# Kernel tuning notes

Measured on AMD Instinct MI355X. Metric: run time of the kernel, lower is better.

Reference implementation:

```python
import jax, jax.numpy as jnp
import numpy as np

N_NODES = 50000
N_EDGES = 800000
N_GRAPHS = 1024
NODE_IN = 128
HID = 300
DEPTH = 5
READOUT = 1024


def setup_inputs() -> dict:
    key = jax.random.key(0)
    ks = jax.random.split(key, 12)
    x = jax.random.normal(ks[0], (N_NODES, NODE_IN), dtype=jnp.float32)
    edge_index = jax.random.randint(ks[1], (2, N_EDGES), 0, N_NODES, dtype=jnp.int32)
    batch = jnp.sort(jax.random.randint(ks[2], (N_NODES,), 0, N_GRAPHS, dtype=jnp.int32))
    s_in = 1.0 / np.sqrt(NODE_IN)
    s_h = 1.0 / np.sqrt(HID)
    W_proj = jax.random.normal(ks[3], (NODE_IN, HID), dtype=jnp.float32) * s_in
    b_proj = jnp.zeros((HID,), dtype=jnp.float32)
    W1 = jax.random.normal(ks[4], (DEPTH, HID, HID), dtype=jnp.float32) * s_h
    b1 = jnp.zeros((DEPTH, HID), dtype=jnp.float32)
    W2 = jax.random.normal(ks[5], (DEPTH, HID, HID), dtype=jnp.float32) * s_h
    b2 = jnp.zeros((DEPTH, HID), dtype=jnp.float32)
    W_sp = jax.random.normal(ks[6], (HID, READOUT), dtype=jnp.float32) * s_h
    b_sp = jnp.zeros((READOUT,), dtype=jnp.float32)
    prelu_a = jnp.full((1,), 0.25, dtype=jnp.float32)  # nn.PReLU default
    return {"x": x, "edge_index": edge_index, "batch": batch,
            "W_proj": W_proj, "b_proj": b_proj, "W1": W1, "b1": b1,
            "W2": W2, "b2": b2, "W_sp": W_sp, "b_sp": b_sp, "prelu_a": prelu_a}


def reference(x, edge_index, batch, W_proj, b_proj, W1, b1, W2, b2, W_sp, b_sp, prelu_a):
    # project_node_feats: Linear + ReLU
    h = jax.nn.relu(x @ W_proj + b_proj)  # [N, HID]
    src = edge_index[0]
    dst = edge_index[1]
    for i in range(DEPTH):
        # GINConv (eps=0): out = nn(x + sum_{j in N(i)} x_j)
        agg = h + jax.ops.segment_sum(h[src], dst, num_segments=N_NODES)
        h = jax.nn.relu(agg @ W1[i] + b1[i]) @ W2[i] + b2[i]
        if i < DEPTH - 1:
            h = jax.nn.relu(h)
        # dropout is identity in eval mode
    # global_add_pool over graph ids
    pooled = jax.ops.segment_sum(h, batch, num_segments=N_GRAPHS)  # [G, HID]
    z = pooled @ W_sp + b_sp  # [G, READOUT]
    # PReLU with single shared parameter
    readout = jnp.where(z >= 0, z, prelu_a[0] * z)
    return readout
```

## Files before the change

### kernel.cpp

```cpp
#include <hip/hip_runtime.h>
#include <cstdint>

#define N_NODES 50000
#define N_EDGES 800000
#define N_GRAPHS 1024
#define NODE_IN 128
#define HID 300
#define DEPTH 5
#define READOUT 1024
#define PSTR 320
#define XSTR 384

typedef float f32x4 __attribute__((ext_vector_type(4)));
typedef short bf16x8 __attribute__((ext_vector_type(8)));
typedef unsigned short us8 __attribute__((ext_vector_type(8)));

__device__ inline unsigned short f2bf(float v) {
    unsigned u = __float_as_uint(v);
    unsigned r = u + 0x7FFFu + ((u >> 16) & 1u);
    return (unsigned short)(r >> 16);
}
__device__ inline float bf2f(unsigned short h) {
    return __uint_as_float((unsigned)h << 16);
}
__device__ inline float bflo(unsigned u) { return __uint_as_float(u << 16); }
__device__ inline float bfhi(unsigned u) { return __uint_as_float(u & 0xFFFF0000u); }
__device__ inline unsigned packbf(float a, float b) {
    return (unsigned)f2bf(a) | ((unsigned)f2bf(b) << 16);
}

__global__ void hist2(const int* __restrict__ dst, int* __restrict__ cnt,
                      const int* __restrict__ batch, int* __restrict__ gcnt) {
    int i = blockIdx.x * blockDim.x + threadIdx.x;
    if (i < N_EDGES) atomicAdd(&cnt[dst[i]], 1);
    else if (i < N_EDGES + N_NODES) atomicAdd(&gcnt[batch[i - N_EDGES]], 1);
}

__global__ __launch_bounds__(256)
void scan_block2(const int* __restrict__ cnt, int* __restrict__ offs, int* __restrict__ bsum,
                 const int* __restrict__ gcnt, int* __restrict__ goffs, int* __restrict__ gsum,
                 int nbn) {
    __shared__ int buf[256];
    int b = blockIdx.x;
    const int* in; int* out; int* bs; int n; int bi;
    if (b < nbn) { in = cnt; out = offs; bs = bsum; n = N_NODES; bi = b; }
    else { in = gcnt; out = goffs; bs = gsum; n = N_GRAPHS; bi = b - nbn; }
    int i = bi * 256 + (int)threadIdx.x;
    int v = (i < n) ? in[i] : 0;
    buf[threadIdx.x] = v;
    __syncthreads();
    for (int off = 1; off < 256; off <<= 1) {
        int t = ((int)threadIdx.x >= off) ? buf[threadIdx.x - off] : 0;
        __syncthreads();
        buf[threadIdx.x] += t;
        __syncthreads();
    }
    if (i < n) out[i] = buf[threadIdx.x] - v;
    if (threadIdx.x == 255) bs[bi] = buf[255];
}

__global__ __launch_bounds__(256)
void scan_base2(const int* __restrict__ bsum, int* __restrict__ bbase, int nbn, int* __restrict__ tot_n,
                const int* __restrict__ gsum, int* __restrict__ gbase, int nbg, int* __restrict__ tot_g) {
    __shared__ int buf[256];
    const int* bs; int* bb; int nb; int* tot;
    if (blockIdx.x == 0) { bs = bsum; bb = bbase; nb = nbn; tot = tot_n; }
    else { bs = gsum; bb = gbase; nb = nbg; tot = tot_g; }
    int v = ((int)threadIdx.x < nb) ? bs[threadIdx.x] : 0;
    buf[threadIdx.x] = v;
    __syncthreads();
    for (int off = 1; off < 256; off <<= 1) {
        int t = ((int)threadIdx.x >= off) ? buf[threadIdx.x - off] : 0;
        __syncthreads();
        buf[threadIdx.x] += t;
        __syncthreads();
    }
    if ((int)threadIdx.x < nb) bb[threadIdx.x] = buf[threadIdx.x] - v;
    if (threadIdx.x == 255) *tot = buf[255];
}

__global__ void scan_add2(int* __restrict__ offs, const int* __restrict__ bbase,
                          int* __restrict__ cursor,
                          int* __restrict__ goffs, const int* __restrict__ gbase, int nbn) {
    int b = blockIdx.x;
    if (b < nbn) {
        int i = b * 256 + (int)threadIdx.x;
        if (i < N_NODES) {
            int o = offs[i] + bbase[b];
            offs[i] = o;
            cursor[i] = o;
        }
    } else {
        int bi = b - nbn;
        int i = bi * 256 + (int)threadIdx.x;
        if (i < N_GRAPHS) goffs[i] += gbase[bi];
    }
}

__global__ void scatter_kernel(const int* __restrict__ src, const int* __restrict__ dst,
                               int* __restrict__ cursor, int* __restrict__ csr, int n) {
    int i = blockIdx.x * blockDim.x + threadIdx.x;
    if (i < n) {
        int p = atomicAdd(&cursor[dst[i]], 1);
        csr[p] = src[i];
    }
}

__global__ __launch_bounds__(256)
void aggregate_bf16(const unsigned short* __restrict__ h, const int* __restrict__ offs,
                    const int* __restrict__ csr, unsigned short* __restrict__ out) {
    int wave = (int)((blockIdx.x * blockDim.x + threadIdx.x) >> 6);
    int lane = threadIdx.x & 63;
    if (wave >= N_NODES) return;
    float a0, a1, a2, a3, a4, a5;
    {
        const unsigned* r = (const unsigned*)(h + (size_t)wave * PSTR);
        uint2 u = *(const uint2*)&r[2 * lane];
        unsigned t = (lane < 32) ? r[128 + lane] : 0u;
        a0 = bflo(u.x); a1 = bfhi(u.x);
        a2 = bflo(u.y); a3 = bfhi(u.y);
        a4 = bflo(t);   a5 = bfhi(t);
    }
    int s = offs[wave], e = offs[wave + 1];
    int k = s;
    for (; k + 3 < e; k += 4) {
        const unsigned* r0 = (const unsigned*)(h + (size_t)csr[k] * PSTR);
        const unsigned* r1 = (const unsigned*)(h + (size_t)csr[k + 1] * PSTR);
        const unsigned* r2 = (const unsigned*)(h + (size_t)csr[k + 2] * PSTR);
        const unsigned* r3 = (const unsigned*)(h + (size_t)csr[k + 3] * PSTR);
        uint2 x0 = *(const uint2*)&r0[2 * lane];
        uint2 x1 = *(const uint2*)&r1[2 * lane];
        uint2 x2 = *(const uint2*)&r2[2 * lane];
        uint2 x3 = *(const uint2*)&r3[2 * lane];
        unsigned t0 = 0, t1 = 0, t2 = 0, t3 = 0;
        if (lane < 32) {
            t0 = r0[128 + lane]; t1 = r1[128 + lane];
            t2 = r2[128 + lane]; t3 = r3[128 + lane];
        }
        a0 += bflo(x0.x) + bflo(x1.x) + bflo(x2.x) + bflo(x3.x);
        a1 += bfhi(x0.x) + bfhi(x1.x) + bfhi(x2.x) + bfhi(x3.x);
        a2 += bflo(x0.y) + bflo(x1.y) + bflo(x2.y) + bflo(x3.y);
        a3 += bfhi(x0.y) + bfhi(x1.y) + bfhi(x2.y) + bfhi(x3.y);
        a4 += bflo(t0) + bflo(t1) + bflo(t2) + bflo(t3);
        a5 += bfhi(t0) + bfhi(t1) + bfhi(t2) + bfhi(t3);
    }
    for (; k < e; ++k) {
        const unsigned* r = (const unsigned*)(h + (size_t)csr[k] * PSTR);
        uint2 u = *(const uint2*)&r[2 * lane];
        unsigned t = (lane < 32) ? r[128 + lane] : 0u;
        a0 += bflo(u.x); a1 += bfhi(u.x);
        a2 += bflo(u.y); a3 += bfhi(u.y);
        a4 += bflo(t);   a5 += bfhi(t);
    }
    unsigned* o = (unsigned*)(out + (size_t)wave * PSTR);
    uint2 w; w.x = packbf(a0, a1); w.y = packbf(a2, a3);
    *(uint2*)&o[2 * lane] = w;
    if (lane < 32) o[128 + lane] = (lane < 22) ? packbf(a4, a5) : 0u;
}

__global__ __launch_bounds__(256)
void split_all(const float* __restrict__ W1, const float* __restrict__ W2,
               const float* __restrict__ Wsp, const float* __restrict__ Wproj,
               unsigned short* __restrict__ w1S, unsigned short* __restrict__ w2S,
               unsigned short* __restrict__ spH, unsigned short* __restrict__ spL,
               unsigned short* __restrict__ Bp) {
    __shared__ float tile[32][33];
    const int STK_SZ = 320 * 640;
    int z = blockIdx.z;
    const float* W;
    int K, N;
    if (z < 10) {
        if (blockIdx.x >= 10) return;
        int l = z % 5;
        W = (z < 5 ? W1 : W2) + (size_t)l * HID * HID;
        K = HID; N = HID;
    } else if (z == 10) {
        W = Wsp; K = HID; N = READOUT;
    } else {
        if (blockIdx.x >= 10 || blockIdx.y >= 4) return;
        W = Wproj; K = NODE_IN; N = HID;
    }
    int n0 = blockIdx.x * 32, k0 = blockIdx.y * 32;
    int tx = threadIdx.x & 31, ty = threadIdx.x >> 5;
#pragma unroll
    for (int r = 0; r < 4; ++r) {
        int k = k0 + ty + r * 8, n = n0 + tx;
        tile[ty + r * 8][tx] = (k < K && n < N) ? W[(size_t)k * N + n] : 0.f;
    }
    __syncthreads();
#pragma unroll
    for (int r = 0; r < 4; ++r) {
        int n = n0 + ty + r * 8, k = k0 + tx;
        float v = tile[tx][ty + r * 8];
        unsigned short hb = f2bf(v);
        unsigned short lb = f2bf(v - bf2f(hb));
        if (z < 10) {
            unsigned short* S = (z < 5 ? w1S : w2S) + (size_t)(z % 5) * STK_SZ;
            S[(size_t)n * 640 + k] = hb;
            S[(size_t)n * 640 + 320 + k] = lb;
        } else if (z == 10) {
            spH[(size_t)n * 320 + k] = hb;
            spL[(size_t)n * 320 + k] = lb;
        } else {
            Bp[(size_t)n * XSTR + k] = hb;
            Bp[(size_t)n * XSTR + 128 + k] = hb;
            Bp[(size_t)n * XSTR + 256 + k] = lb;
        }
    }
}

__global__ void split_x(const float* __restrict__ x, unsigned short* __restrict__ xs) {
    int i = blockIdx.x * blockDim.x + threadIdx.x;
    if (i >= N_NODES * 64) return;
    int row = i >> 6, c = i & 63;
    float2 v = *(const float2*)&x[(size_t)row * NODE_IN + 2 * c];
    unsigned short h0 = f2bf(v.x), h1 = f2bf(v.y);
    unsigned short l0 = f2bf(v.x - bf2f(h0)), l1 = f2bf(v.y - bf2f(h1));
    unsigned hp = (unsigned)h0 | ((unsigned)h1 << 16);
    unsigned lp = (unsigned)l0 | ((unsigned)l1 << 16);
    unsigned* o = (unsigned*)(xs + (size_t)row * XSTR);
    o[c] = hp;
    o[64 + c] = lp;
    o[128 + c] = hp;
}

#define BSWZ(r, c) ((c) ^ (((r) >> 1) & 3))

__global__ __launch_bounds__(256, 2)
void gin_mlp64(const unsigned short* __restrict__ Ap, int M,
               const unsigned short* __restrict__ B1, const float* __restrict__ b1,
               const unsigned short* __restrict__ B2, const float* __restrict__ b2,
               unsigned short* __restrict__ Op, int act2) {
    __shared__ __align__(16) unsigned short At[64 * 320];
    __shared__ __align__(16) unsigned short Bs[2 * 10240];

    const int tid = threadIdx.x;
    const int bm = blockIdx.x * 64;
    const int wn = tid >> 6, lane = tid & 63;
    const int lr = lane & 15, lk = lane >> 4;

    float b1v[5], b2v[5];
#pragma unroll
    for (int n = 0; n < 5; ++n) {
        int col = wn * 80 + n * 16 + lr;
        b1v[n] = (col < HID) ? b1[col] : 0.f;
        b2v[n] = (col < HID) ? b2[col] : 0.f;
    }

    size_t bofs[10]; int bldso[10];
#pragma unroll
    for (int i = 0; i < 10; ++i) {
        int q = i * 256 + tid;
        int half = q >= 1280;
        int q2 = q - half * 1280;
        int r = q2 >> 2, c = q2 & 3;
        bofs[i] = (size_t)r * 640 + half * 320 + c * 8;
        bldso[i] = half * 10240 + r * 32 + BSWZ(r, c) * 8;
    }

    us8 vB[10];
    auto LOADB = [&](const unsigned short* B, int t) {
        int k0 = t * 32;
#pragma unroll
        for (int i = 0; i < 10; ++i)
            vB[i] = *(const us8*)&B[bofs[i] + k0];
    };

    LOADB(B1, 0);

#pragma unroll
    for (int i = 0; i < 10; ++i) {
        int g = i * 256 + tid;
        int row = g / 40, c = g - row * 40;
        int grow = bm + row; if (grow >= M) grow = M - 1;
        us8 v = *(const us8*)&Ap[(size_t)grow * PSTR + c * 8];
        *(us8*)&At[row * 320 + (c ^ (row & 7)) * 8] = v;
    }

    f32x4 acc[4][5];

    auto RUN = [&](const unsigned short* B) {
        for (int t = 0; t < 10; ++t) {
            __syncthreads();
#pragma unroll
            for (int i = 0; i < 10; ++i) *(us8*)&Bs[bldso[i]] = vB[i];
            if (t < 9) LOADB(B, t + 1);
            __syncthreads();
            bf16x8 aS[4];
            int ac = t * 4 + lk;
#pragma unroll
            for (int m = 0; m < 4; ++m) {
                int row = m * 16 + lr;
                aS[m] = *(const bf16x8*)&At[row * 320 + (ac ^ (row & 7)) * 8];
            }
#pragma unroll
            for (int n = 0; n < 5; ++n) {
                int rb = wn * 80 + n * 16 + lr;
                int sc = rb * 32 + BSWZ(rb, lk) * 8;
                bf16x8 bh = *(const bf16x8*)&Bs[sc];
                bf16x8 bl = *(const bf16x8*)&Bs[10240 + sc];
#pragma unroll
                for (int m = 0; m < 4; ++m) {
                    acc[m][n] = __builtin_amdgcn_mfma_f32_16x16x32_bf16(aS[m], bh, acc[m][n], 0, 0, 0);
                    acc[m][n] = __builtin_amdgcn_mfma_f32_16x16x32_bf16(aS[m], bl, acc[m][n], 0, 0, 0);
                }
            }
        }
    };

#pragma unroll
    for (int m = 0; m < 4; ++m)
#pragma unroll
        for (int n = 0; n < 5; ++n) acc[m][n] = (f32x4)0.f;
    RUN(B1);

    LOADB(B2, 0);

    __syncthreads();
#pragma unroll
    for (int n = 0; n < 5; ++n) {
        int col = wn * 80 + n * 16 + lr;
        int cc = col >> 3, cp = col & 7;
        float bv = b1v[n];
        bool vc = col < HID;
#pragma unroll
        for (int m = 0; m < 4; ++m) {
#pragma unroll
            for (int p = 0; p < 4; ++p) {
                int row = m * 16 + lk * 4 + p;
                float v = vc ? fmaxf(acc[m][n][p] + bv, 0.f) : 0.f;
                At[row * 320 + ((cc ^ (row & 7)) * 8) + cp] = f2bf(v);
            }
        }
    }

#pragma unroll
    for (int m = 0; m < 4; ++m)
#pragma unroll
        for (int n = 0; n < 5; ++n) acc[m][n] = (f32x4)0.f;
    RUN(B2);

    __syncthreads();
#pragma unroll
    for (int n = 0; n < 5; ++n) {
        int col = wn * 80 + n * 16 + lr;
        int cc = col >> 3, cp = col & 7;
        float bv = b2v[n];
        bool vc = col < HID;
#pragma unroll
        for (int m = 0; m < 4; ++m) {
#pragma unroll
            for (int p = 0; p < 4; ++p) {
                int row = m * 16 + lk * 4 + p;
                float v = vc ? (acc[m][n][p] + bv) : 0.f;
                if (act2) v = fmaxf(v, 0.f);
                At[row * 320 + ((cc ^ (row & 7)) * 8) + cp] = f2bf(v);
            }
        }
    }
    __syncthreads();
#pragma unroll
    for (int i = 0; i < 10; ++i) {
        int g = i * 256 + tid;
        int row = g / 40, c = g - row * 40;
        int grow = bm + row;
        if (grow < M)
            *(us8*)&Op[(size_t)grow * PSTR + c * 8] =
                *(const us8*)&At[row * 320 + (c ^ (row & 7)) * 8];
    }
}

template<int NPL>
__global__ __launch_bounds__(512)
void gemm_plane4(const unsigned short* __restrict__ Ap, int astr, int M, int KP,
                 const unsigned short* __restrict__ BH, const unsigned short* __restrict__ BL,
                 const float* __restrict__ bias, unsigned short* __restrict__ Op, int act) {
    constexpr int BITER = (NPL * 1280 + 511) / 512;
    __shared__ __align__(16) unsigned short As[2][256 * 40];
    __shared__ __align__(16) unsigned short Bs[2][NPL * 10240];

    const int tid = threadIdx.x;
    const int bm = blockIdx.x * 256;
    const int wid = tid >> 6, lane = tid & 63;
    const int wm = wid >> 2, wn = wid & 3;
    const int lr = lane & 15, lk = lane >> 4;
    const int arow = tid >> 1, ach = (tid & 1) * 2;
    int agr = bm + arow; if (agr >= M) agr = M - 1;
    const unsigned short* aSrc = Ap + (size_t)agr * astr + ach * 8;

    const unsigned short* bsrc[BITER];
    int bldso[BITER];
    bool bval[BITER];
#pragma unroll
    for (int i = 0; i < BITER; ++i) {
        int qq = i * 512 + tid;
        bval[i] = qq < NPL * 1280;
        int p = (NPL == 2 && qq >= 1280) ? 1 : 0;
        int q2 = qq - p * 1280;
        int r = q2 >> 2, c = q2 & 3;
        const unsigned short* base = p ? BL : BH;
        bsrc[i] = base + (size_t)r * KP + c * 8;
        bldso[i] = p * 10240 + r * 32 + BSWZ(r, c) * 8;
    }

    f32x4 acc[8][5];
#pragma unroll
    for (int m = 0; m < 8; ++m)
#pragma unroll
        for (int n = 0; n < 5; ++n) acc[m][n] = (f32x4)0.f;

    us8 vA0, vA1, vB[BITER];
    auto LOADS = [&](int t) {
        int k0 = t * 32;
        vA0 = *(const us8*)&aSrc[k0];
        vA1 = *(const us8*)&aSrc[k0 + 8];
#pragma unroll
        for (int i = 0; i < BITER; ++i)
            if (bval[i]) vB[i] = *(const us8*)&bsrc[i][k0];
    };
    auto WRITE = [&](int b) {
        *(us8*)&As[b][arow * 40 + ach * 8] = vA0;
        *(us8*)&As[b][arow * 40 + ach * 8 + 8] = vA1;
#pragma unroll
        for (int i = 0; i < BITER; ++i)
            if (bval[i]) *(us8*)&Bs[b][bldso[i]] = vB[i];
    };

    const int nt = KP / 32;
    LOADS(0);
    WRITE(0);
    int buf = 0;
    for (int t = 0; t < nt; ++t) {
        bool more = (t + 1 < nt);
        if (more) LOADS(t + 1);
        __syncthreads();
        bf16x8 aS[8];
#pragma unroll
        for (int m = 0; m < 8; ++m)
            aS[m] = *(const bf16x8*)&As[buf][(wm * 128 + m * 16 + lr) * 40 + lk * 8];
#pragma unroll
        for (int n = 0; n < 5; ++n) {
            int rb = wn * 80 + n * 16 + lr;
            int sc = rb * 32 + BSWZ(rb, lk) * 8;
            bf16x8 bh = *(const bf16x8*)&Bs[buf][sc];
#pragma unroll
            for (int m = 0; m < 8; ++m)
                acc[m][n] = __builtin_amdgcn_mfma_f32_16x16x32_bf16(aS[m], bh, acc[m][n], 0, 0, 0);
            if (NPL == 2) {
                bf16x8 bl = *(const bf16x8*)&Bs[buf][10240 + sc];
#pragma unroll
                for (int m = 0; m < 8; ++m)
                    acc[m][n] = __builtin_amdgcn_mfma_f32_16x16x32_bf16(aS[m], bl, acc[m][n], 0, 0, 0);
            }
        }
        if (more) WRITE(buf ^ 1);
        buf ^= 1;
    }
#pragma unroll
    for (int n = 0; n < 5; ++n) {
        int col = wn * 80 + n * 16 + lr;
        bool vc = col < HID;
        float bv = vc ? bias[col] : 0.f;
#pragma unroll
        for (int m = 0; m < 8; ++m) {
            int rbase = bm + wm * 128 + m * 16 + lk * 4;
#pragma unroll
            for (int p = 0; p < 4; ++p) {
                int row = rbase + p;
                if (row >= M) continue;
                float v = vc ? (acc[m][n][p] + bv) : 0.f;
                if (act == 1) v = fmaxf(v, 0.f);
                Op[(size_t)row * PSTR + col] = f2bf(v);
            }
        }
    }
}

__global__ __launch_bounds__(256)
void gemm_f32A(const float* __restrict__ A, int lda, int M, int K, int KP,
               const unsigned short* __restrict__ BH, const unsigned short* __restrict__ BL, int KPB,
               const float* __restrict__ bias, int N,
               float* __restrict__ C, int ldc, int act, const float* __restrict__ prelu) {
    __shared__ __align__(16) unsigned short AsH[64 * 40];
    __shared__ __align__(16) unsigned short AsL[64 * 40];
    __shared__ __align__(16) unsigned short BsH[320 * 40];
    __shared__ __align__(16) unsigned short BsL[320 * 40];

    const int tid = threadIdx.x;
    const int bm = blockIdx.y * 64;
    const int bn = blockIdx.x * 320;
    const int wid = tid >> 6, lane = tid & 63;
    const int lr = lane & 15, lk = lane >> 4;
    const int ar = tid >> 2, ac = tid & 3;

    f32x4 acc[4][5];
#pragma unroll
    for (int m = 0; m < 4; ++m)
#pragma unroll
        for (int n = 0; n < 5; ++n) acc[m][n] = (f32x4)0.f;

    for (int k0 = 0; k0 < KP; k0 += 32) {
        {
            int gm = bm + ar;
            int k = k0 + ac * 8;
            float v[8];
#pragma unroll
            for (int j = 0; j < 8; ++j) v[j] = 0.f;
            if (gm < M) {
                if (k + 7 < K) {
                    float4 p0 = *(const float4*)&A[(size_t)gm * lda + k];
                    float4 p1 = *(const float4*)&A[(size_t)gm * lda + k + 4];
                    v[0] = p0.x; v[1] = p0.y; v[2] = p0.z; v[3] = p0.w;
                    v[4] = p1.x; v[5] = p1.y; v[6] = p1.z; v[7] = p1.w;
                } else {
#pragma unroll
                    for (int j = 0; j < 8; ++j)
                        if (k + j < K) v[j] = A[(size_t)gm * lda + k + j];
                }
            }
            us8 h, l;
#pragma unroll
            for (int j = 0; j < 8; ++j) {
                unsigned short hb = f2bf(v[j]);
                h[j] = hb;
                l[j] = f2bf(v[j] - bf2f(hb));
            }
            *(us8*)&AsH[ar * 40 + ac * 8] = h;
            *(us8*)&AsL[ar * 40 + ac * 8] = l;
        }
#pragma unroll
        for (int p = 0; p < 5; ++p) {
            int r = ar + p * 64;
            size_t gb = (size_t)(bn + r) * KPB + k0 + ac * 8;
            *(us8*)&BsH[r * 40 + ac * 8] = *(const us8*)&BH[gb];
            *(us8*)&BsL[r * 40 + ac * 8] = *(const us8*)&BL[gb];
        }
        __syncthreads();
        bf16x8 aH[4], aL[4];
#pragma unroll
        for (int m = 0; m < 4; ++m) {
            aH[m] = *(const bf16x8*)&AsH[(m * 16 + lr) * 40 + lk * 8];
            aL[m] = *(const bf16x8*)&AsL[(m * 16 + lr) * 40 + lk * 8];
        }
#pragma unroll
        for (int n = 0; n < 5; ++n) {
            int r = wid * 80 + n * 16 + lr;
            bf16x8 bh = *(const bf16x8*)&BsH[r * 40 + lk * 8];
            bf16x8 bl = *(const bf16x8*)&BsL[r * 40 + lk * 8];
#pragma unroll
            for (int m = 0; m < 4; ++m) {
                acc[m][n] = __builtin_amdgcn_mfma_f32_16x16x32_bf16(aH[m], bh, acc[m][n], 0, 0, 0);
                acc[m][n] = __builtin_amdgcn_mfma_f32_16x16x32_bf16(aH[m], bl, acc[m][n], 0, 0, 0);
                acc[m][n] = __builtin_amdgcn_mfma_f32_16x16x32_bf16(aL[m], bh, acc[m][n], 0, 0, 0);
            }
        }
        __syncthreads();
    }
    float slope = (act == 2) ? prelu[0] : 0.f;
#pragma unroll
    for (int n = 0; n < 5; ++n) {
        int col = bn + wid * 80 + n * 16 + lr;
        bool vc = col < N;
        float bv = vc ? bias[col] : 0.f;
#pragma unroll
        for (int m = 0; m < 4; ++m) {
            int rbase = bm + m * 16 + lk * 4;
#pragma unroll
            for (int p = 0; p < 4; ++p) {
                int row = rbase + p;
                if (row >= M) continue;
                float v = vc ? (acc[m][n][p] + bv) : 0.f;
                if (act == 1) v = fmaxf(v, 0.f);
                else if (act == 2) v = (v >= 0.f) ? v : slope * v;
                if (vc) C[(size_t)row * ldc + col] = v;
            }
        }
    }
}

__global__ __launch_bounds__(128)
void pool_seg(const unsigned short* __restrict__ h, const int* __restrict__ goffs,
              float* __restrict__ pooled) {
    __shared__ float red[6 * 64];
    int g = blockIdx.x;
    int w = threadIdx.x >> 6, lane = threadIdx.x & 63;
    int s = goffs[g], e = goffs[g + 1];
    float a0 = 0.f, a1 = 0.f, a2 = 0.f, a3 = 0.f, a4 = 0.f, a5 = 0.f;
    for (int node = s + w; node < e; node += 2) {
        const unsigned* r = (const unsigned*)(h + (size_t)node * PSTR);
        uint2 u = *(const uint2*)&r[2 * lane];
        unsigned t = (lane < 32) ? r[128 + lane] : 0u;
        a0 += bflo(u.x); a1 += bfhi(u.x);
        a2 += bflo(u.y); a3 += bfhi(u.y);
        a4 += bflo(t);   a5 += bfhi(t);
    }
    if (w == 1) {
        red[lane] = a0;        red[64 + lane] = a1;
        red[128 + lane] = a2;  red[192 + lane] = a3;
        red[256 + lane] = a4;  red[320 + lane] = a5;
    }
    __syncthreads();
    if (w == 0) {
        a0 += red[lane];        a1 += red[64 + lane];
        a2 += red[128 + lane];  a3 += red[192 + lane];
        a4 += red[256 + lane];  a5 += red[320 + lane];
        float* pr = pooled + (size_t)g * PSTR;
        *(float4*)&pr[4 * lane] = make_float4(a0, a1, a2, a3);
        if (lane < 32) *(float2*)&pr[256 + 2 * lane] = make_float2(a4, a5);
    }
}

extern "C" void kernel_launch(void* const* d_in, const int* in_sizes, int n_in,
                              void* d_out, int out_size, void* d_ws, size_t ws_size,
                              hipStream_t stream) {
    const float* x      = (const float*)d_in[0];
    const int*   eidx   = (const int*)d_in[1];
    const int*   batch  = (const int*)d_in[2];
    const float* W_proj = (const float*)d_in[3];
    const float* b_proj = (const float*)d_in[4];
    const float* W1     = (const float*)d_in[5];
    const float* b1     = (const float*)d_in[6];
    const float* W2     = (const float*)d_in[7];
    const float* b2     = (const float*)d_in[8];
    const float* W_sp   = (const float*)d_in[9];
    const float* b_sp   = (const float*)d_in[10];
    const float* prelu  = (const float*)d_in[11];

    const int* src = eidx;
    const int* dst = eidx + N_EDGES;

    const size_t PLANE  = (size_t)N_NODES * PSTR + 64;
    const size_t XPLANE = (size_t)N_NODES * XSTR + 64;
    const int STK_SZ = 320 * 640;
    const int SP_SZ  = 1280 * 320;
    const int BP_SZ  = 320 * XSTR;
    const int NB  = (N_NODES + 255) / 256;
    const int NBG = (N_GRAPHS + 255) / 256;

    unsigned short* hA  = (unsigned short*)d_ws;
    unsigned short* hBx = hA + PLANE;
    unsigned short* xs  = hBx;
    float* pooled = (float*)(hBx + XPLANE);
    unsigned short* w1S = (unsigned short*)(pooled + (size_t)N_GRAPHS * PSTR + 16);
    unsigned short* w2S = w1S + 5 * (size_t)STK_SZ;
    unsigned short* spH = w2S + 5 * (size_t)STK_SZ;
    unsigned short* spL = spH + SP_SZ;
    unsigned short* Bp  = spL + SP_SZ;
    int* cnt    = (int*)(((uintptr_t)(Bp + BP_SZ) + 15) & ~(uintptr_t)15);
    int* gcnt   = cnt + N_NODES;
    int* bsum   = gcnt + N_GRAPHS;
    int* bbase  = bsum + 256;
    int* gsum   = bbase + 256;
    int* gbase  = gsum + 256;
    int* offs   = gbase + 256;
    int* goffs  = offs + N_NODES + 1;
    int* cursor = goffs + N_GRAPHS + 1;
    int* csr    = cursor + N_NODES;
    size_t needed = (size_t)((uintptr_t)(csr + N_EDGES) - (uintptr_t)d_ws);
    if (ws_size < needed) return;

    split_all<<<dim3(40, 10, 12), 256, 0, stream>>>(W1, W2, W_sp, W_proj,
                                                    w1S, w2S, spH, spL, Bp);
    split_x<<<(N_NODES * 64 + 255) / 256, 256, 0, stream>>>(x, xs);

    hipMemsetAsync(cnt, 0, (N_NODES + N_GRAPHS) * sizeof(int), stream);
    hist2<<<(N_EDGES + N_NODES + 255) / 256, 256, 0, stream>>>(dst, cnt, batch, gcnt);
    scan_block2<<<NB + NBG, 256, 0, stream>>>(cnt, offs, bsum, gcnt, goffs, gsum, NB);
    scan_base2<<<2, 256, 0, stream>>>(bsum, bbase, NB, offs + N_NODES,
                                      gsum, gbase, NBG, goffs + N_GRAPHS);
    scan_add2<<<NB + NBG, 256, 0, stream>>>(offs, bbase, cursor, goffs, gbase, NB);
    scatter_kernel<<<(N_EDGES + 255) / 256, 256, 0, stream>>>(src, dst, cursor, csr, N_EDGES);

    gemm_plane4<1><<<(N_NODES + 255) / 256, 512, 0, stream>>>(
        xs, XSTR, N_NODES, XSTR, Bp, nullptr, b_proj, hA, 1);

    const int GBM = (N_NODES + 63) / 64;
    unsigned short* cur = hA;
    unsigned short* agp = hBx;
    for (int i = 0; i < DEPTH; ++i) {
        aggregate_bf16<<<(N_NODES * 64 + 255) / 256, 256, 0, stream>>>(cur, offs, csr, agp);
        gin_mlp64<<<GBM, 256, 0, stream>>>(
            agp, N_NODES,
            w1S + (size_t)i * STK_SZ, b1 + (size_t)i * HID,
            w2S + (size_t)i * STK_SZ, b2 + (size_t)i * HID,
            cur, (i < DEPTH - 1) ? 1 : 0);
    }

    pool_seg<<<N_GRAPHS, 128, 0, stream>>>(cur, goffs, pooled);

    gemm_f32A<<<dim3(4, (N_GRAPHS + 63) / 64), 256, 0, stream>>>(
        pooled, PSTR, N_GRAPHS, HID, 320, spH, spL, 320,
        b_sp, READOUT, (float*)d_out, READOUT, 2, prelu);
}
```

Baseline: 1.031 ms.

## Enlarge GIN MLP tile to 128 rows and fuse fp32 projection GEMM

The fused GIN MLP kernel now handles 128 rows per block with 512 threads (8 waves in a 2x4 layout) and uses a K-step of 64 with a new XOR swizzle. Each weight tile loaded into LDS is therefore reused across twice as many rows, and the kernel needs fewer barriers. Separately, the input projection now reuses the fp32-A split GEMM directly on x, which removes the split_x preprocessing kernel and the padded x plane, and the GEMM gains a bf16 plane output mode. The larger LDS footprint (about 160KB) allows only one block per CU, which may hurt latency hiding, and the projection GEMM now uses a 64-row tile.

```diff
diff --git a/kernel.cpp b/kernel.cpp
--- a/kernel.cpp
+++ b/kernel.cpp
@@ -9,7 +9,6 @@
 #define DEPTH 5
 #define READOUT 1024
 #define PSTR 320
-#define XSTR 384
 
 typedef float f32x4 __attribute__((ext_vector_type(4)));
 typedef short bf16x8 __attribute__((ext_vector_type(8)));
@@ -163,7 +162,7 @@
                const float* __restrict__ Wsp, const float* __restrict__ Wproj,
                unsigned short* __restrict__ w1S, unsigned short* __restrict__ w2S,
                unsigned short* __restrict__ spH, unsigned short* __restrict__ spL,
-               unsigned short* __restrict__ Bp) {
+               unsigned short* __restrict__ pjH, unsigned short* __restrict__ pjL) {
     __shared__ float tile[32][33];
     const int STK_SZ = 320 * 640;
     int z = blockIdx.z;
@@ -202,41 +201,26 @@
             spH[(size_t)n * 320 + k] = hb;
             spL[(size_t)n * 320 + k] = lb;
         } else {
-            Bp[(size_t)n * XSTR + k] = hb;
-            Bp[(size_t)n * XSTR + 128 + k] = hb;
-            Bp[(size_t)n * XSTR + 256 + k] = lb;
-        }
-    }
-}
-
-__global__ void split_x(const float* __restrict__ x, unsigned short* __restrict__ xs) {
-    int i = blockIdx.x * blockDim.x + threadIdx.x;
-    if (i >= N_NODES * 64) return;
-    int row = i >> 6, c = i & 63;
-    float2 v = *(const float2*)&x[(size_t)row * NODE_IN + 2 * c];
-    unsigned short h0 = f2bf(v.x), h1 = f2bf(v.y);
-    unsigned short l0 = f2bf(v.x - bf2f(h0)), l1 = f2bf(v.y - bf2f(h1));
-    unsigned hp = (unsigned)h0 | ((unsigned)h1 << 16);
-    unsigned lp = (unsigned)l0 | ((unsigned)l1 << 16);
-    unsigned* o = (unsigned*)(xs + (size_t)row * XSTR);
-    o[c] = hp;
-    o[64 + c] = lp;
-    o[128 + c] = hp;
+            pjH[(size_t)n * 128 + k] = hb;
+            pjL[(size_t)n * 128 + k] = lb;
+        }
+    }
 }
 
 #define BSWZ(r, c) ((c) ^ (((r) >> 1) & 3))
 
-__global__ __launch_bounds__(256, 2)
-void gin_mlp64(const unsigned short* __restrict__ Ap, int M,
-               const unsigned short* __restrict__ B1, const float* __restrict__ b1,
-               const unsigned short* __restrict__ B2, const float* __restrict__ b2,
-               unsigned short* __restrict__ Op, int act2) {
-    __shared__ __align__(16) unsigned short At[64 * 320];
-    __shared__ __align__(16) unsigned short Bs[2 * 10240];
+__global__ __launch_bounds__(512, 1)
+void gin_mlp_bk64(const unsigned short* __restrict__ Ap, int M,
+                  const unsigned short* __restrict__ B1, const float* __restrict__ b1,
+                  const unsigned short* __restrict__ B2, const float* __restrict__ b2,
+                  unsigned short* __restrict__ Op, int act2) {
+    __shared__ __align__(16) unsigned short At[128 * 320];
+    __shared__ __align__(16) unsigned short Bs[2 * 320 * 64];
 
     const int tid = threadIdx.x;
-    const int bm = blockIdx.x * 64;
-    const int wn = tid >> 6, lane = tid & 63;
+    const int bm = blockIdx.x * 128;
+    const int wid = tid >> 6, lane = tid & 63;
+    const int wm = wid >> 2, wn = wid & 3;
     const int lr = lane & 15, lk = lane >> 4;
 
     float b1v[5], b2v[5];
@@ -250,17 +234,17 @@
     size_t bofs[10]; int bldso[10];
 #pragma unroll
     for (int i = 0; i < 10; ++i) {
-        int q = i * 256 + tid;
-        int half = q >= 1280;
-        int q2 = q - half * 1280;
-        int r = q2 >> 2, c = q2 & 3;
+        int q = i * 512 + tid;
+        int half = q >= 2560;
+        int q2 = q - half * 2560;
+        int r = q2 >> 3, c = q2 & 7;
         bofs[i] = (size_t)r * 640 + half * 320 + c * 8;
-        bldso[i] = half * 10240 + r * 32 + BSWZ(r, c) * 8;
+        bldso[i] = half * 20480 + r * 64 + ((c ^ (r & 7)) * 8);
     }
 
     us8 vB[10];
     auto LOADB = [&](const unsigned short* B, int t) {
-        int k0 = t * 32;
+        int k0 = t * 64;
 #pragma unroll
         for (int i = 0; i < 10; ++i)
             vB[i] = *(const us8*)&B[bofs[i] + k0];
@@ -270,7 +254,7 @@
 
 #pragma unroll
     for (int i = 0; i < 10; ++i) {
-        int g = i * 256 + tid;
+        int g = i * 512 + tid;
         int row = g / 40, c = g - row * 40;
         int grow = bm + row; if (grow >= M) grow = M - 1;
         us8 v = *(const us8*)&Ap[(size_t)grow * PSTR + c * 8];
@@ -280,29 +264,33 @@
     f32x4 acc[4][5];
 
     auto RUN = [&](const unsigned short* B) {
-        for (int t = 0; t < 10; ++t) {
+        for (int t = 0; t < 5; ++t) {
             __syncthreads();
 #pragma unroll
             for (int i = 0; i < 10; ++i) *(us8*)&Bs[bldso[i]] = vB[i];
-            if (t < 9) LOADB(B, t + 1);
+            if (t < 4) LOADB(B, t + 1);
             __syncthreads();
-            bf16x8 aS[4];
-            int ac = t * 4 + lk;
-#pragma unroll
-            for (int m = 0; m < 4; ++m) {
-                int row = m * 16 + lr;
-                aS[m] = *(const bf16x8*)&At[row * 320 + (ac ^ (row & 7)) * 8];
-            }
-#pragma unroll
-            for (int n = 0; n < 5; ++n) {
-                int rb = wn * 80 + n * 16 + lr;
-                int sc = rb * 32 + BSWZ(rb, lk) * 8;
-                bf16x8 bh = *(const bf16x8*)&Bs[sc];
-                bf16x8 bl = *(const bf16x8*)&Bs[10240 + sc];
+#pragma unroll
+            for (int kk = 0; kk < 2; ++kk) {
+                bf16x8 aS[4];
+                int ac = t * 8 + kk * 4 + lk;
 #pragma unroll
                 for (int m = 0; m < 4; ++m) {
-                    acc[m][n] = __builtin_amdgcn_mfma_f32_16x16x32_bf16(aS[m], bh, acc[m][n], 0, 0, 0);
-                    acc[m][n] = __builtin_amdgcn_mfma_f32_16x16x32_bf16(aS[m], bl, acc[m][n], 0, 0, 0);
+                    int row = wm * 64 + m * 16 + lr;
+                    aS[m] = *(const bf16x8*)&At[row * 320 + (ac ^ (row & 7)) * 8];
+                }
+                int bc = kk * 4 + lk;
+#pragma unroll
+                for (int n = 0; n < 5; ++n) {
+                    int rb = wn * 80 + n * 16 + lr;
+                    int so = rb * 64 + ((bc ^ (rb & 7)) * 8);
+                    bf16x8 bh = *(const bf16x8*)&Bs[so];
+                    bf16x8 bl = *(const bf16x8*)&Bs[20480 + so];
+#pragma unroll
+                    for (int m = 0; m < 4; ++m) {
+                        acc[m][n] = __builtin_amdgcn_mfma_f32_16x16x32_bf16(aS[m], bh, acc[m][n], 0, 0, 0);
+                        acc[m][n] = __builtin_amdgcn_mfma_f32_16x16x32_bf16(aS[m], bl, acc[m][n], 0, 0, 0);
+                    }
                 }
             }
         }
@@ -327,7 +315,7 @@
         for (int m = 0; m < 4; ++m) {
 #pragma unroll
             for (int p = 0; p < 4; ++p) {
-                int row = m * 16 + lk * 4 + p;
+                int row = wm * 64 + m * 16 + lk * 4 + p;
                 float v = vc ? fmaxf(acc[m][n][p] + bv, 0.f) : 0.f;
                 At[row * 320 + ((cc ^ (row & 7)) * 8) + cp] = f2bf(v);
             }
@@ -351,7 +339,7 @@
         for (int m = 0; m < 4; ++m) {
 #pragma unroll
             for (int p = 0; p < 4; ++p) {
-                int row = m * 16 + lk * 4 + p;
+                int row = wm * 64 + m * 16 + lk * 4 + p;
                 float v = vc ? (acc[m][n][p] + bv) : 0.f;
                 if (act2) v = fmaxf(v, 0.f);
                 At[row * 320 + ((cc ^ (row & 7)) * 8) + cp] = f2bf(v);
@@ -361,7 +349,7 @@
     __syncthreads();
 #pragma unroll
     for (int i = 0; i < 10; ++i) {
-        int g = i * 256 + tid;
+        int g = i * 512 + tid;
         int row = g / 40, c = g - row * 40;
         int grow = bm + row;
         if (grow < M)
@@ -370,117 +358,12 @@
     }
 }
 
-template<int NPL>
-__global__ __launch_bounds__(512)
-void gemm_plane4(const unsigned short* __restrict__ Ap, int astr, int M, int KP,
-                 const unsigned short* __restrict__ BH, const unsigned short* __restrict__ BL,
-                 const float* __restrict__ bias, unsigned short* __restrict__ Op, int act) {
-    constexpr int BITER = (NPL * 1280 + 511) / 512;
-    __shared__ __align__(16) unsigned short As[2][256 * 40];
-    __shared__ __align__(16) unsigned short Bs[2][NPL * 10240];
-
-    const int tid = threadIdx.x;
-    const int bm = blockIdx.x * 256;
-    const int wid = tid >> 6, lane = tid & 63;
-    const int wm = wid >> 2, wn = wid & 3;
-    const int lr = lane & 15, lk = lane >> 4;
-    const int arow = tid >> 1, ach = (tid & 1) * 2;
-    int agr = bm + arow; if (agr >= M) agr = M - 1;
-    const unsigned short* aSrc = Ap + (size_t)agr * astr + ach * 8;
-
-    const unsigned short* bsrc[BITER];
-    int bldso[BITER];
-    bool bval[BITER];
-#pragma unroll
-    for (int i = 0; i < BITER; ++i) {
-        int qq = i * 512 + tid;
-        bval[i] = qq < NPL * 1280;
-        int p = (NPL == 2 && qq >= 1280) ? 1 : 0;
-        int q2 = qq - p * 1280;
-        int r = q2 >> 2, c = q2 & 3;
-        const unsigned short* base = p ? BL : BH;
-        bsrc[i] = base + (size_t)r * KP + c * 8;
-        bldso[i] = p * 10240 + r * 32 + BSWZ(r, c) * 8;
-    }
-
-    f32x4 acc[8][5];
-#pragma unroll
-    for (int m = 0; m < 8; ++m)
-#pragma unroll
-        for (int n = 0; n < 5; ++n) acc[m][n] = (f32x4)0.f;
-
-    us8 vA0, vA1, vB[BITER];
-    auto LOADS = [&](int t) {
-        int k0 = t * 32;
-        vA0 = *(const us8*)&aSrc[k0];
-        vA1 = *(const us8*)&aSrc[k0 + 8];
-#pragma unroll
-        for (int i = 0; i < BITER; ++i)
-            if (bval[i]) vB[i] = *(const us8*)&bsrc[i][k0];
-    };
-    auto WRITE = [&](int b) {
-        *(us8*)&As[b][arow * 40 + ach * 8] = vA0;
-        *(us8*)&As[b][arow * 40 + ach * 8 + 8] = vA1;
-#pragma unroll
-        for (int i = 0; i < BITER; ++i)
-            if (bval[i]) *(us8*)&Bs[b][bldso[i]] = vB[i];
-    };
-
-    const int nt = KP / 32;
-    LOADS(0);
-    WRITE(0);
-    int buf = 0;
-    for (int t = 0; t < nt; ++t) {
-        bool more = (t + 1 < nt);
-        if (more) LOADS(t + 1);
-        __syncthreads();
-        bf16x8 aS[8];
-#pragma unroll
-        for (int m = 0; m < 8; ++m)
-            aS[m] = *(const bf16x8*)&As[buf][(wm * 128 + m * 16 + lr) * 40 + lk * 8];
-#pragma unroll
-        for (int n = 0; n < 5; ++n) {
-            int rb = wn * 80 + n * 16 + lr;
-            int sc = rb * 32 + BSWZ(rb, lk) * 8;
-            bf16x8 bh = *(const bf16x8*)&Bs[buf][sc];
-#pragma unroll
-            for (int m = 0; m < 8; ++m)
-                acc[m][n] = __builtin_amdgcn_mfma_f32_16x16x32_bf16(aS[m], bh, acc[m][n], 0, 0, 0);
-            if (NPL == 2) {
-                bf16x8 bl = *(const bf16x8*)&Bs[buf][10240 + sc];
-#pragma unroll
-                for (int m = 0; m < 8; ++m)
-                    acc[m][n] = __builtin_amdgcn_mfma_f32_16x16x32_bf16(aS[m], bl, acc[m][n], 0, 0, 0);
-            }
-        }
-        if (more) WRITE(buf ^ 1);
-        buf ^= 1;
-    }
-#pragma unroll
-    for (int n = 0; n < 5; ++n) {
-        int col = wn * 80 + n * 16 + lr;
-        bool vc = col < HID;
-        float bv = vc ? bias[col] : 0.f;
-#pragma unroll
-        for (int m = 0; m < 8; ++m) {
-            int rbase = bm + wm * 128 + m * 16 + lk * 4;
-#pragma unroll
-            for (int p = 0; p < 4; ++p) {
-                int row = rbase + p;
-                if (row >= M) continue;
-                float v = vc ? (acc[m][n][p] + bv) : 0.f;
-                if (act == 1) v = fmaxf(v, 0.f);
-                Op[(size_t)row * PSTR + col] = f2bf(v);
-            }
-        }
-    }
-}
-
 __global__ __launch_bounds__(256)
 void gemm_f32A(const float* __restrict__ A, int lda, int M, int K, int KP,
                const unsigned short* __restrict__ BH, const unsigned short* __restrict__ BL, int KPB,
                const float* __restrict__ bias, int N,
-               float* __restrict__ C, int ldc, int act, const float* __restrict__ prelu) {
+               float* __restrict__ C, int ldc, unsigned short* __restrict__ Op, int outPlane,
+               int act, const float* __restrict__ prelu) {
     __shared__ __align__(16) unsigned short AsH[64 * 40];
     __shared__ __align__(16) unsigned short AsL[64 * 40];
     __shared__ __align__(16) unsigned short BsH[320 * 40];
@@ -572,7 +455,11 @@
                 float v = vc ? (acc[m][n][p] + bv) : 0.f;
                 if (act == 1) v = fmaxf(v, 0.f);
                 else if (act == 2) v = (v >= 0.f) ? v : slope * v;
-                if (vc) C[(size_t)row * ldc + col] = v;
+                if (outPlane) {
+                    if (col < PSTR) Op[(size_t)row * PSTR + col] = f2bf(v);
+                } else if (vc) {
+                    C[(size_t)row * ldc + col] = v;
+                }
             }
         }
     }
@@ -629,24 +516,23 @@
     const int* src = eidx;
     const int* dst = eidx + N_EDGES;
 
-    const size_t PLANE  = (size_t)N_NODES * PSTR + 64;
-    const size_t XPLANE = (size_t)N_NODES * XSTR + 64;
+    const size_t PLANE = (size_t)N_NODES * PSTR + 64;
     const int STK_SZ = 320 * 640;
     const int SP_SZ  = 1280 * 320;
-    const int BP_SZ  = 320 * XSTR;
+    const int PJ_SZ  = 320 * 128;
     const int NB  = (N_NODES + 255) / 256;
     const int NBG = (N_GRAPHS + 255) / 256;
 
     unsigned short* hA  = (unsigned short*)d_ws;
-    unsigned short* hBx = hA + PLANE;
-    unsigned short* xs  = hBx;
-    float* pooled = (float*)(hBx + XPLANE);
+    unsigned short* hB  = hA + PLANE;
+    float* pooled = (float*)(hB + PLANE);
     unsigned short* w1S = (unsigned short*)(pooled + (size_t)N_GRAPHS * PSTR + 16);
     unsigned short* w2S = w1S + 5 * (size_t)STK_SZ;
     unsigned short* spH = w2S + 5 * (size_t)STK_SZ;
     unsigned short* spL = spH + SP_SZ;
-    unsigned short* Bp  = spL + SP_SZ;
-    int* cnt    = (int*)(((uintptr_t)(Bp + BP_SZ) + 15) & ~(uintptr_t)15);
+    unsigned short* pjH = spL + SP_SZ;
+    unsigned short* pjL = pjH + PJ_SZ;
+    int* cnt    = (int*)(((uintptr_t)(pjL + PJ_SZ) + 15) & ~(uintptr_t)15);
     int* gcnt   = cnt + N_NODES;
     int* bsum   = gcnt + N_GRAPHS;
     int* bbase  = bsum + 256;
@@ -660,8 +546,7 @@
     if (ws_size < needed) return;
 
     split_all<<<dim3(40, 10, 12), 256, 0, stream>>>(W1, W2, W_sp, W_proj,
-                                                    w1S, w2S, spH, spL, Bp);
-    split_x<<<(N_NODES * 64 + 255) / 256, 256, 0, stream>>>(x, xs);
+                                                    w1S, w2S, spH, spL, pjH, pjL);
 
     hipMemsetAsync(cnt, 0, (N_NODES + N_GRAPHS) * sizeof(int), stream);
     hist2<<<(N_EDGES + N_NODES + 255) / 256, 256, 0, stream>>>(dst, cnt, batch, gcnt);
@@ -671,15 +556,16 @@
     scan_add2<<<NB + NBG, 256, 0, stream>>>(offs, bbase, cursor, goffs, gbase, NB);
     scatter_kernel<<<(N_EDGES + 255) / 256, 256, 0, stream>>>(src, dst, cursor, csr, N_EDGES);
 
-    gemm_plane4<1><<<(N_NODES + 255) / 256, 512, 0, stream>>>(
-        xs, XSTR, N_NODES, XSTR, Bp, nullptr, b_proj, hA, 1);
-
-    const int GBM = (N_NODES + 63) / 64;
+    gemm_f32A<<<dim3(1, (N_NODES + 63) / 64), 256, 0, stream>>>(
+        x, NODE_IN, N_NODES, NODE_IN, 128, pjH, pjL, 128,
+        b_proj, HID, nullptr, 0, hA, 1, 1, nullptr);
+
+    const int GBM = (N_NODES + 127) / 128;
     unsigned short* cur = hA;
-    unsigned short* agp = hBx;
+    unsigned short* agp = hB;
     for (int i = 0; i < DEPTH; ++i) {
         aggregate_bf16<<<(N_NODES * 64 + 255) / 256, 256, 0, stream>>>(cur, offs, csr, agp);
-        gin_mlp64<<<GBM, 256, 0, stream>>>(
+        gin_mlp_bk64<<<GBM, 512, 0, stream>>>(
             agp, N_NODES,
             w1S + (size_t)i * STK_SZ, b1 + (size_t)i * HID,
             w2S + (size_t)i * STK_SZ, b2 + (size_t)i * HID,
@@ -690,5 +576,5 @@
 
     gemm_f32A<<<dim3(4, (N_GRAPHS + 63) / 64), 256, 0, stream>>>(
         pooled, PSTR, N_GRAPHS, HID, 320, spH, spL, 320,
-        b_sp, READOUT, (float*)d_out, READOUT, 2, prelu);
-}
+        b_sp, READOUT, (float*)d_out, READOUT, nullptr, 0, 2, prelu);
+}
```

Measured after the change: 1.033 ms. No clear change (+0.2%).
